# Kernel optimization log

Hardware: AMD Instinct MI355X
Metric: run time of the kernel (lower is better)

The kernel has to match this reference:

```python
import jax, jax.numpy as jnp
import numpy as np
from jax import lax

B, C_IN, C_OUT, H, W, K, PAD = 4, 64, 64, 96, 96, 3, 1
K2 = K * K


def setup_inputs() -> dict:
    key = jax.random.key(0)
    k1, k2, k3, k4, k5 = jax.random.split(key, 5)
    x = jax.random.normal(k1, (B, C_IN, H, W), jnp.float32)
    offset = jax.random.normal(k2, (B, 2 * K2, H, W), jnp.float32)
    weight = jax.random.normal(k3, (C_OUT, C_IN, K, K), jnp.float32) * 0.05
    mask_weight = jax.random.normal(k4, (K2, C_IN, K, K), jnp.float32) * 0.05
    mask_bias = jax.random.normal(k5, (K2,), jnp.float32) * 0.05
    return {"x": x, "offset": offset, "weight": weight,
            "mask_weight": mask_weight, "mask_bias": mask_bias}


def _deform_conv2d(x, offset, weight, mask):
    # torchvision ordering: per kernel tap k, offset[:, 2k] is dy, offset[:, 2k+1] is dx
    off_y = offset[:, 0::2]  # [B, K2, H, W]
    off_x = offset[:, 1::2]
    ky, kx = jnp.meshgrid(jnp.arange(K), jnp.arange(K), indexing="ij")
    ky = ky.reshape(K2).astype(x.dtype)
    kx = kx.reshape(K2).astype(x.dtype)
    hh = jnp.arange(H, dtype=x.dtype)
    ww = jnp.arange(W, dtype=x.dtype)
    base_y = hh[None, :, None] - PAD + ky[:, None, None]   # [K2, H, 1]
    base_x = ww[None, None, :] - PAD + kx[:, None, None]   # [K2, 1, W]
    py = base_y[None] + off_y                               # [B, K2, H, W]
    px = base_x[None] + off_x

    y0 = jnp.floor(py)
    x0 = jnp.floor(px)
    wy = py - y0   # bilinear weights
    wx = px - x0
    y0i = y0.astype(jnp.int32)
    x0i = x0.astype(jnp.int32)

    x_flat = x.reshape(B, C_IN, H * W)

    def gather(yy, xx):
        valid = (yy >= 0) & (yy < H) & (xx >= 0) & (xx < W)
        idx = jnp.clip(yy, 0, H - 1) * W + jnp.clip(xx, 0, W - 1)  # [B,K2,H,W]
        idx_f = idx.reshape(B, -1)
        v = jax.vmap(lambda xf, i: xf[:, i])(x_flat, idx_f)  # [B, C, K2*H*W]
        v = v.reshape(B, C_IN, K2, H, W)
        return v * valid[:, None].astype(v.dtype)

    v00 = gather(y0i, x0i)
    v01 = gather(y0i, x0i + 1)
    v10 = gather(y0i + 1, x0i)
    v11 = gather(y0i + 1, x0i + 1)

    wy_ = wy[:, None]  # [B,1,K2,H,W]
    wx_ = wx[:, None]
    sampled = (v00 * (1 - wy_) * (1 - wx_) + v01 * (1 - wy_) * wx_
               + v10 * wy_ * (1 - wx_) + v11 * wy_ * wx_)
    sampled = sampled * mask[:, None]  # modulate by sigmoid mask

    w2 = weight.reshape(C_OUT, C_IN, K2)
    return jnp.einsum("bckhw,ock->bohw", sampled, w2)


def reference(x, offset, weight, mask_weight, mask_bias):
    mask_logits = lax.conv_general_dilated(
        x, mask_weight, window_strides=(1, 1), padding=[(PAD, PAD), (PAD, PAD)],
        dimension_numbers=("NCHW", "OIHW", "NCHW"))
    mask = jax.nn.sigmoid(mask_logits + mask_bias[None, :, None, None])
    return _deform_conv2d(x, offset, weight, mask)
```

## Files before the change

### kernel.cpp

```cpp
#include <hip/hip_runtime.h>
#include <hip/hip_bf16.h>
#include <math.h>

#define BB 4
#define CI 64
#define CO 64
#define HH 96
#define WW 96
#define HW (HH*WW)
#define K2 9
#define PADC 1

#define TW 4
#define TH 4
#define TPXT 16
#define TBX (WW/TW)
#define TBY (HH/TH)
#define SLEN 3
#define GRID 768

#define WC 16
#define SREC 70
#define NSLOT (16*WC)

typedef __attribute__((ext_vector_type(8))) short short8;
typedef __attribute__((ext_vector_type(4))) float float4v;
typedef __attribute__((ext_vector_type(4))) unsigned int uint4v;

#define WF_USHORTS (18*64*32)
#define MWF_USHORTS (18*16*32)

__device__ __forceinline__ short f2bf(float f) {
    unsigned int u = __float_as_uint(f);
    u = (u + 0x7fffu + ((u >> 16) & 1u)) >> 16;
    return (short)u;
}
__device__ __forceinline__ unsigned int pkbf(float lo, float hi) {
    float2 f; f.x = lo; f.y = hi;
    union { __hip_bfloat162 h; unsigned int u; } z;
    z.h = __float22bfloat162_rn(f);
    return z.u;
}

__global__ __launch_bounds__(256) void pack_kernel(const float* __restrict__ wgt,
                                                   const float* __restrict__ mw,
                                                   unsigned short* __restrict__ Wf,
                                                   unsigned short* __restrict__ MWf) {
    int i = blockIdx.x * 256 + threadIdx.x;
    if (i < WF_USHORTS) {
        int frag = i >> 11;
        int o = (i >> 5) & 63;
        int tt = i & 31;
        int k = frag >> 1, cc = frag & 1;
        int c = cc * 32 + tt;
        Wf[i] = (unsigned short)f2bf(wgt[o * 576 + c * 9 + k]);
    } else if (i < WF_USHORTS + MWF_USHORTS) {
        int e = i - WF_USHORTS;
        int frag = e >> 9;
        int m = (e >> 5) & 15;
        int tt = e & 31;
        int q = frag >> 1, cc = frag & 1;
        int c = cc * 32 + tt;
        MWf[e] = (m < 9) ? (unsigned short)f2bf(mw[m * 576 + c * 9 + q]) : 0;
    }
}

struct SmemT {
    unsigned short win[NSLOT * SREC];
    float mred[2][2][K2][TPXT];
    int   idx[K2][4][TPXT];
    float w[K2][4][TPXT];
    float part[2][16][64];
};

__device__ __forceinline__ uint4v ld_win4(const unsigned int* w32, int dw) {
    uint4v z;
    z[0] = w32[dw + 0]; z[1] = w32[dw + 1];
    z[2] = w32[dw + 2]; z[3] = w32[dw + 3];
    return z;
}
__device__ __forceinline__ short8 ld_win8(const unsigned int* w32, int dw) {
    union { uint4v u; short8 s; } z;
    z.u = ld_win4(w32, dw);
    return z.s;
}

__device__ __forceinline__ void stage_load(const float* __restrict__ xb, int label,
                                           int chp, int c0c, float4v* a, float4v* bq) {
    int row = min(max(label, 0), HH - 1);
    const float* s0 = xb + (size_t)(2 * chp) * HW + row * WW;
    const float* s1 = s0 + HW;
    if (c0c >= 0 && c0c + 3 < WW) {
        *a = *(const float4v*)(s0 + c0c);
        *bq = *(const float4v*)(s1 + c0c);
    } else {
        #pragma unroll
        for (int j = 0; j < 4; j++) {
            int cc2 = min(max(c0c + j, 0), WW - 1);
            (*a)[j] = s0[cc2]; (*bq)[j] = s1[cc2];
        }
    }
}
__device__ __forceinline__ void stage_write(unsigned int* w32, int label, int chp,
                                            int c4, float4v a, float4v bq) {
    int rslot = (label & 15) * WC;
    #pragma unroll
    for (int j = 0; j < 4; j++)
        w32[(rslot + c4 * 4 + j) * 35 + chp] = pkbf(a[j], bq[j]);
}

template<int KB, int KE>
__device__ __forceinline__ void run_strip(SmemT& sm, int t, int wv, int ch, int tg,
                                          const float* __restrict__ x,
                                          const float* __restrict__ off,
                                          const float* __restrict__ mbias,
                                          const unsigned short* __restrict__ Wf,
                                          const unsigned short* __restrict__ MWf,
                                          float* __restrict__ out, int bid) {
    constexpr int NK = KE - KB;
    int lane = t & 63;
    int n = lane & 15, quad = lane >> 4;
    unsigned int* w32 = (unsigned int*)sm.win;
    const unsigned int* w32c = (const unsigned int*)sm.win;

    int g = bid & 7, r = bid >> 3;
    int b = g & 3, txh = g >> 2;
    int col = r >> 3, s = r & 7;
    int tx = txh * 12 + col;
    int ty0 = s * SLEN;
    int w0 = tx * TW;
    int wc0 = w0 - 4;
    const float* xb = x + (size_t)b * CI * HW;

    short8 wA[NK][4];
    short8 mA[NK];
    #pragma unroll
    for (int kk = 0; kk < NK; kk++) {
        int k = KB + kk;
        const unsigned short* wp = Wf + (size_t)((k * 2 + ch) * 64) * 32 + quad * 8;
        #pragma unroll
        for (int ss = 0; ss < 4; ss++)
            wA[kk][ss] = *(const short8*)(wp + (ss * 16 + n) * 32);
        mA[kk] = *(const short8*)(MWf + ((size_t)((k * 2 + ch) * 16 + n)) * 32 + quad * 8);
    }

    int ly = n >> 2, lx = n & 3;
    int cbase_dw = ch * 16 + quad * 4;

    for (int e = t; e < 13 * 128; e += 256) {
        int ri = e >> 7, chp = (e >> 2) & 31, c4 = e & 3;
        float4v a, bq;
        stage_load(xb, ty0 * TH - 4 + ri, chp, wc0 + c4 * 4, &a, &bq);
        stage_write(w32, ty0 * TH - 4 + ri, chp, c4, a, bq);
    }
    bool bm = t < K2 * TPXT;
    int km = t >> 4, pem = t & 15;
    float mbr = 0.f;
    size_t offy_base = ((size_t)b * 2 * K2 + 2 * km) * HW;
    size_t offx_base = offy_base + HW;
    float poy = 0.f, pox = 0.f;
    if (bm) {
        mbr = mbias[km];
        int p = (ty0 * TH + (pem >> 2)) * WW + w0 + (pem & 3);
        poy = off[offy_base + p];
        pox = off[offx_base + p];
    }

    for (int j = 0; j < SLEN; j++) {
        int h0 = (ty0 + j) * TH;
        int h = h0 + ly, wcc = w0 + lx;
        __syncthreads();

        float4v pa0, pb0, pa1, pb1;
        float noy = 0.f, nox = 0.f;
        bool hn = (j + 1 < SLEN);
        if (hn) {
            int e1 = t + 256;
            stage_load(xb, h0 + 9 + (t >> 7), (t >> 2) & 31, wc0 + (t & 3) * 4, &pa0, &pb0);
            stage_load(xb, h0 + 9 + (e1 >> 7), (e1 >> 2) & 31, wc0 + (e1 & 3) * 4, &pa1, &pb1);
            if (bm) {
                int p = (h0 + 4 + (pem >> 2)) * WW + w0 + (pem & 3);
                noy = off[offy_base + p];
                nox = off[offx_base + p];
            }
        }

        {
            float4v macc = {0.f, 0.f, 0.f, 0.f};
            #pragma unroll
            for (int kk = 0; kk < NK; kk++) {
                int q = KB + kk;
                int hh = h + q / 3 - 1, ww2 = wcc + q % 3 - 1;
                bool valid = (hh >= 0) && (hh < HH) && (ww2 >= 0) && (ww2 < WW);
                short8 bfrag = {0, 0, 0, 0, 0, 0, 0, 0};
                if (valid) {
                    int slot = (hh & 15) * WC + (ww2 - wc0);
                    bfrag = ld_win8(w32c, slot * 35 + cbase_dw);
                }
                macc = __builtin_amdgcn_mfma_f32_16x16x32_bf16(mA[kk], bfrag, macc, 0, 0, 0);
            }
            #pragma unroll
            for (int rr = 0; rr < 4; rr++) {
                int row = quad * 4 + rr;
                if (row < 9) sm.mred[ch][tg][row][n] = macc[rr];
            }
        }
        __syncthreads();

        if (bm) {
            int ph = h0 + (pem >> 2), pw = w0 + (pem & 3);
            float sl = sm.mred[0][0][km][pem] + sm.mred[0][1][km][pem] +
                       sm.mred[1][0][km][pem] + sm.mred[1][1][km][pem] + mbr;
            float m = 1.f / (1.f + expf(-sl));
            float py  = (float)(ph - PADC + km / 3) + poy;
            float pxf = (float)(pw - PADC + km % 3) + pox;
            float y0f = floorf(py), x0f = floorf(pxf);
            float wy = py - y0f, wx = pxf - x0f;
            int y0 = (int)y0f, x0 = (int)x0f;
            int y1 = y0 + 1, x1 = x0 + 1;
            int y0c = min(max(y0, 0), HH - 1), y1c = min(max(y1, 0), HH - 1);
            int x0c = min(max(x0, 0), WW - 1), x1c = min(max(x1, 0), WW - 1);
            bool vy0 = (y0 >= 0) && (y0 < HH), vy1 = (y1 >= 0) && (y1 < HH);
            bool vx0 = (x0 >= 0) && (x0 < WW), vx1 = (x1 >= 0) && (x1 < WW);
            float w00 = (1.f - wy) * (1.f - wx) * m; if (!(vy0 && vx0)) w00 = 0.f;
            float w01 = (1.f - wy) * wx * m;         if (!(vy0 && vx1)) w01 = 0.f;
            float w10 = wy * (1.f - wx) * m;         if (!(vy1 && vx0)) w10 = 0.f;
            float w11 = wy * wx * m;                 if (!(vy1 && vx1)) w11 = 0.f;
            sm.idx[km][0][pem] = (y0c << 16) | x0c;
            sm.idx[km][1][pem] = (y0c << 16) | x1c;
            sm.idx[km][2][pem] = (y1c << 16) | x0c;
            sm.idx[km][3][pem] = (y1c << 16) | x1c;
            sm.w[km][0][pem] = w00; sm.w[km][1][pem] = w01;
            sm.w[km][2][pem] = w10; sm.w[km][3][pem] = w11;
        }
        __syncthreads();

        float4v acc0 = {0.f, 0.f, 0.f, 0.f};
        float4v acc1 = {0.f, 0.f, 0.f, 0.f};
        float4v acc2 = {0.f, 0.f, 0.f, 0.f};
        float4v acc3 = {0.f, 0.f, 0.f, 0.f};
        const float* xfb = xb + (size_t)(ch * 32 + quad * 8) * HW;

        #pragma unroll
        for (int kk = 0; kk < NK; kk++) {
            int k = KB + kk;
            uint4v U[4];
            #pragma unroll
            for (int cor = 0; cor < 4; cor++) {
                int yx = sm.idx[k][cor][n];
                int yy = yx >> 16, xx = yx & 0xffff;
                bool inw = (yy >= h0 - 4) && (yy <= h0 + 8) &&
                           (xx >= wc0) && (xx <= wc0 + 15);
                uint4v u;
                if (inw) {
                    int slot = (yy & 15) * WC + (xx - wc0);
                    u = ld_win4(w32c, slot * 35 + cbase_dw);
                } else {
                    const float* fs = xfb + yy * WW + xx;
                    #pragma unroll
                    for (int dd = 0; dd < 4; dd++)
                        u[dd] = pkbf(fs[(size_t)(2 * dd) * HW], fs[(size_t)(2 * dd + 1) * HW]);
                }
                U[cor] = u;
            }
            float w0v = sm.w[k][0][n], w1v = sm.w[k][1][n];
            float w2v = sm.w[k][2][n], w3v = sm.w[k][3][n];
            union { unsigned int u[4]; short8 s; } bf;
            #pragma unroll
            for (int dd = 0; dd < 4; dd++) {
                float lo = __uint_as_float(U[0][dd] << 16) * w0v
                         + __uint_as_float(U[1][dd] << 16) * w1v
                         + __uint_as_float(U[2][dd] << 16) * w2v
                         + __uint_as_float(U[3][dd] << 16) * w3v;
                float hi = __uint_as_float(U[0][dd] & 0xffff0000u) * w0v
                         + __uint_as_float(U[1][dd] & 0xffff0000u) * w1v
                         + __uint_as_float(U[2][dd] & 0xffff0000u) * w2v
                         + __uint_as_float(U[3][dd] & 0xffff0000u) * w3v;
                bf.u[dd] = pkbf(lo, hi);
            }
            acc0 = __builtin_amdgcn_mfma_f32_16x16x32_bf16(wA[kk][0], bf.s, acc0, 0, 0, 0);
            acc1 = __builtin_amdgcn_mfma_f32_16x16x32_bf16(wA[kk][1], bf.s, acc1, 0, 0, 0);
            acc2 = __builtin_amdgcn_mfma_f32_16x16x32_bf16(wA[kk][2], bf.s, acc2, 0, 0, 0);
            acc3 = __builtin_amdgcn_mfma_f32_16x16x32_bf16(wA[kk][3], bf.s, acc3, 0, 0, 0);
        }

        if (wv >= 2) {
            #pragma unroll
            for (int rr = 0; rr < 4; rr++) {
                sm.part[wv - 2][0 * 4 + rr][lane] = acc0[rr];
                sm.part[wv - 2][1 * 4 + rr][lane] = acc1[rr];
                sm.part[wv - 2][2 * 4 + rr][lane] = acc2[rr];
                sm.part[wv - 2][3 * 4 + rr][lane] = acc3[rr];
            }
        }
        __syncthreads();
        if (wv == 1) {
            #pragma unroll
            for (int rr = 0; rr < 4; rr++) {
                acc0[rr] += sm.part[1][0 * 4 + rr][lane];
                acc1[rr] += sm.part[1][1 * 4 + rr][lane];
                acc2[rr] += sm.part[1][2 * 4 + rr][lane];
                acc3[rr] += sm.part[1][3 * 4 + rr][lane];
            }
            #pragma unroll
            for (int rr = 0; rr < 4; rr++) {
                sm.part[1][0 * 4 + rr][lane] = acc0[rr];
                sm.part[1][1 * 4 + rr][lane] = acc1[rr];
                sm.part[1][2 * 4 + rr][lane] = acc2[rr];
                sm.part[1][3 * 4 + rr][lane] = acc3[rr];
            }
        }
        if (wv == 0) {
            #pragma unroll
            for (int rr = 0; rr < 4; rr++) {
                acc0[rr] += sm.part[0][0 * 4 + rr][lane];
                acc1[rr] += sm.part[0][1 * 4 + rr][lane];
                acc2[rr] += sm.part[0][2 * 4 + rr][lane];
                acc3[rr] += sm.part[0][3 * 4 + rr][lane];
            }
        }
        __syncthreads();
        if (wv == 0) {
            float* ob = out + (size_t)b * CO * HW + h * WW + wcc;
            #pragma unroll
            for (int rr = 0; rr < 4; rr++) {
                ob[(size_t)(0 * 16 + quad * 4 + rr) * HW] = acc0[rr] + sm.part[1][0 * 4 + rr][lane];
                ob[(size_t)(1 * 16 + quad * 4 + rr) * HW] = acc1[rr] + sm.part[1][1 * 4 + rr][lane];
                ob[(size_t)(2 * 16 + quad * 4 + rr) * HW] = acc2[rr] + sm.part[1][2 * 4 + rr][lane];
                ob[(size_t)(3 * 16 + quad * 4 + rr) * HW] = acc3[rr] + sm.part[1][3 * 4 + rr][lane];
            }
        }

        if (hn) {
            int e1 = t + 256;
            stage_write(w32, h0 + 9 + (t >> 7), (t >> 2) & 31, t & 3, pa0, pb0);
            stage_write(w32, h0 + 9 + (e1 >> 7), (e1 >> 2) & 31, e1 & 3, pa1, pb1);
            poy = noy; pox = nox;
        }
    }
}

__global__ __launch_bounds__(256, 3) void fused_kernel(const float* __restrict__ x,
                                                       const float* __restrict__ off,
                                                       const float* __restrict__ mbias,
                                                       const unsigned short* __restrict__ Wf,
                                                       const unsigned short* __restrict__ MWf,
                                                       float* __restrict__ out) {
    __shared__ SmemT sm;
    int t = threadIdx.x;
    int wv = t >> 6;
    int ch = wv & 1, tg = wv >> 1;
    if (tg == 0)
        run_strip<0, 5>(sm, t, wv, ch, tg, x, off, mbias, Wf, MWf, out, blockIdx.x);
    else
        run_strip<5, 9>(sm, t, wv, ch, tg, x, off, mbias, Wf, MWf, out, blockIdx.x);
}

extern "C" void kernel_launch(void* const* d_in, const int* in_sizes, int n_in,
                              void* d_out, int out_size, void* d_ws, size_t ws_size,
                              hipStream_t stream) {
    const float* x   = (const float*)d_in[0];
    const float* off = (const float*)d_in[1];
    const float* wgt = (const float*)d_in[2];
    const float* mw  = (const float*)d_in[3];
    const float* mb  = (const float*)d_in[4];
    float* out = (float*)d_out;

    unsigned short* Wf  = (unsigned short*)d_ws;
    unsigned short* MWf = Wf + WF_USHORTS;

    hipLaunchKernelGGL(pack_kernel, dim3((WF_USHORTS + MWF_USHORTS + 255) / 256), dim3(256),
                       0, stream, wgt, mw, Wf, MWf);
    hipLaunchKernelGGL(fused_kernel, dim3(GRID), dim3(256), 0, stream,
                       x, off, mb, Wf, MWf, out);
}
```

Baseline: 108.1 us.

## Lengthen row strips, double-buffer partial sums, cut reduction barrier

Each block now walks strips of 5 (or 4) tile-rows, so the grid drops from 768 to 480 blocks and more of the staged input window is reused along each strip. The cross-wave reduction is reworked: waves 1-3 write partials into a double-buffered shared array and wave 0 sums all three, which removes one __syncthreads per row and the serial two-stage reduction. Launch bounds drop from 3 to 2 blocks per CU, giving each thread more registers but lowering occupancy. The 480-block grid with uneven strip lengths may load-balance worse across CUs.

```diff
diff --git a/kernel.cpp b/kernel.cpp
--- a/kernel.cpp
+++ b/kernel.cpp
@@ -16,8 +16,7 @@
 #define TPXT 16
 #define TBX (WW/TW)
 #define TBY (HH/TH)
-#define SLEN 3
-#define GRID 768
+#define GRID 480
 
 #define WC 16
 #define SREC 70
@@ -70,7 +69,7 @@
     float mred[2][2][K2][TPXT];
     int   idx[K2][4][TPXT];
     float w[K2][4][TPXT];
-    float part[2][16][64];
+    float part[2][3][16][64];
 };
 
 __device__ __forceinline__ uint4v ld_win4(const unsigned int* w32, int dw) {
@@ -125,9 +124,10 @@
 
     int g = bid & 7, r = bid >> 3;
     int b = g & 3, txh = g >> 2;
-    int col = r >> 3, s = r & 7;
+    int col = r / 5, s = r % 5;
     int tx = txh * 12 + col;
-    int ty0 = s * SLEN;
+    int ty0 = (s < 4) ? s * 5 : 20;
+    int len = (s < 4) ? 5 : 4;
     int w0 = tx * TW;
     int wc0 = w0 - 4;
     const float* xb = x + (size_t)b * CI * HW;
@@ -166,14 +166,15 @@
         pox = off[offx_base + p];
     }
 
-    for (int j = 0; j < SLEN; j++) {
+    for (int j = 0; j < len; j++) {
         int h0 = (ty0 + j) * TH;
         int h = h0 + ly, wcc = w0 + lx;
+        int pb = j & 1;
         __syncthreads();
 
         float4v pa0, pb0, pa1, pb1;
         float noy = 0.f, nox = 0.f;
-        bool hn = (j + 1 < SLEN);
+        bool hn = (j + 1 < len);
         if (hn) {
             int e1 = t + 256;
             stage_load(xb, h0 + 9 + (t >> 7), (t >> 2) & 31, wc0 + (t & 3) * 4, &pa0, &pb0);
@@ -284,39 +285,13 @@
             acc3 = __builtin_amdgcn_mfma_f32_16x16x32_bf16(wA[kk][3], bf.s, acc3, 0, 0, 0);
         }
 
-        if (wv >= 2) {
+        if (wv != 0) {
             #pragma unroll
             for (int rr = 0; rr < 4; rr++) {
-                sm.part[wv - 2][0 * 4 + rr][lane] = acc0[rr];
-                sm.part[wv - 2][1 * 4 + rr][lane] = acc1[rr];
-                sm.part[wv - 2][2 * 4 + rr][lane] = acc2[rr];
-                sm.part[wv - 2][3 * 4 + rr][lane] = acc3[rr];
-            }
-        }
-        __syncthreads();
-        if (wv == 1) {
-            #pragma unroll
-            for (int rr = 0; rr < 4; rr++) {
-                acc0[rr] += sm.part[1][0 * 4 + rr][lane];
-                acc1[rr] += sm.part[1][1 * 4 + rr][lane];
-                acc2[rr] += sm.part[1][2 * 4 + rr][lane];
-                acc3[rr] += sm.part[1][3 * 4 + rr][lane];
-            }
-            #pragma unroll
-            for (int rr = 0; rr < 4; rr++) {
-                sm.part[1][0 * 4 + rr][lane] = acc0[rr];
-                sm.part[1][1 * 4 + rr][lane] = acc1[rr];
-                sm.part[1][2 * 4 + rr][lane] = acc2[rr];
-                sm.part[1][3 * 4 + rr][lane] = acc3[rr];
-            }
-        }
-        if (wv == 0) {
-            #pragma unroll
-            for (int rr = 0; rr < 4; rr++) {
-                acc0[rr] += sm.part[0][0 * 4 + rr][lane];
-                acc1[rr] += sm.part[0][1 * 4 + rr][lane];
-                acc2[rr] += sm.part[0][2 * 4 + rr][lane];
-                acc3[rr] += sm.part[0][3 * 4 + rr][lane];
+                sm.part[pb][wv - 1][0 * 4 + rr][lane] = acc0[rr];
+                sm.part[pb][wv - 1][1 * 4 + rr][lane] = acc1[rr];
+                sm.part[pb][wv - 1][2 * 4 + rr][lane] = acc2[rr];
+                sm.part[pb][wv - 1][3 * 4 + rr][lane] = acc3[rr];
             }
         }
         __syncthreads();
@@ -324,10 +299,15 @@
             float* ob = out + (size_t)b * CO * HW + h * WW + wcc;
             #pragma unroll
             for (int rr = 0; rr < 4; rr++) {
-                ob[(size_t)(0 * 16 + quad * 4 + rr) * HW] = acc0[rr] + sm.part[1][0 * 4 + rr][lane];
-                ob[(size_t)(1 * 16 + quad * 4 + rr) * HW] = acc1[rr] + sm.part[1][1 * 4 + rr][lane];
-                ob[(size_t)(2 * 16 + quad * 4 + rr) * HW] = acc2[rr] + sm.part[1][2 * 4 + rr][lane];
-                ob[(size_t)(3 * 16 + quad * 4 + rr) * HW] = acc3[rr] + sm.part[1][3 * 4 + rr][lane];
+                int j0 = rr, j1 = 4 + rr, j2 = 8 + rr, j3 = 12 + rr;
+                ob[(size_t)(0 * 16 + quad * 4 + rr) * HW] = acc0[rr] +
+                    sm.part[pb][0][j0][lane] + sm.part[pb][1][j0][lane] + sm.part[pb][2][j0][lane];
+                ob[(size_t)(1 * 16 + quad * 4 + rr) * HW] = acc1[rr] +
+                    sm.part[pb][0][j1][lane] + sm.part[pb][1][j1][lane] + sm.part[pb][2][j1][lane];
+                ob[(size_t)(2 * 16 + quad * 4 + rr) * HW] = acc2[rr] +
+                    sm.part[pb][0][j2][lane] + sm.part[pb][1][j2][lane] + sm.part[pb][2][j2][lane];
+                ob[(size_t)(3 * 16 + quad * 4 + rr) * HW] = acc3[rr] +
+                    sm.part[pb][0][j3][lane] + sm.part[pb][1][j3][lane] + sm.part[pb][2][j3][lane];
             }
         }
 
@@ -340,7 +320,7 @@
     }
 }
 
-__global__ __launch_bounds__(256, 3) void fused_kernel(const float* __restrict__ x,
+__global__ __launch_bounds__(256, 2) void fused_kernel(const float* __restrict__ x,
                                                        const float* __restrict__ off,
                                                        const float* __restrict__ mbias,
                                                        const unsigned short* __restrict__ Wf,
```

Measured after the change: 105.7 us. 2.2% less time.
